# Optimization experiments

Measured on AMD Instinct MI355X. Metric: run time of the kernel, lower is better.

## Reference

```python
import jax, jax.numpy as jnp
import numpy as np

N = 16384
E = 524288
F_IN, F_HID, F_OUT = 128, 256, 128
EPS = 1e-5


def setup_inputs() -> dict:
    key = jax.random.key(0)
    ks = jax.random.split(key, 8)
    x = jax.random.normal(ks[0], (N, F_IN), dtype=jnp.float32)
    edge_index = jax.random.randint(ks[1], (2, E), 0, N, dtype=jnp.int64)
    edge_weight = jax.random.uniform(ks[2], (E,), dtype=jnp.float32)
    # Linear params stored as [in, out] (y = x @ W + b; same math as torch Linear)
    W1_w = jax.random.normal(ks[3], (F_IN, F_HID), dtype=jnp.float32) / np.sqrt(F_IN)
    W1_b = jnp.zeros((F_HID,), dtype=jnp.float32)
    W2_w = jax.random.normal(ks[4], (F_HID, F_OUT), dtype=jnp.float32) / np.sqrt(F_HID)
    W2_b = jnp.zeros((F_OUT,), dtype=jnp.float32)
    ln_g = jnp.ones((F_HID,), dtype=jnp.float32)
    ln_b = jnp.zeros((F_HID,), dtype=jnp.float32)
    return {"x": x, "edge_index": edge_index, "edge_weight": edge_weight,
            "W1_w": W1_w, "W1_b": W1_b, "W2_w": W2_w, "W2_b": W2_b,
            "ln_g": ln_g, "ln_b": ln_b}


def _layernorm(h, g, b):
    mu = jnp.mean(h, axis=-1, keepdims=True)
    var = jnp.var(h, axis=-1, keepdims=True)
    return (h - mu) * jax.lax.rsqrt(var + EPS) * g + b


def reference(x, edge_index, edge_weight, W1_w, W1_b, W2_w, W2_b, ln_g, ln_b):
    n = x.shape[0]
    adj = jnp.zeros((n, n), dtype=x.dtype).at[edge_index[0], edge_index[1]].set(edge_weight)
    adj = adj + jnp.eye(n, dtype=x.dtype)
    degree = jnp.clip(adj.sum(axis=1, keepdims=True), 1.0, None)
    adj = adj / degree
    h = jnp.matmul(adj, x) @ W1_w + W1_b          # [N, F_HID]
    h = jax.nn.relu(_layernorm(h, ln_g, ln_b))
    # dropout is identity in eval mode
    out = jnp.matmul(adj, h) @ W2_w + W2_b        # [N, F_OUT]
    return out
```

## Files before the change

### kernel.cpp

```cpp
#include <hip/hip_runtime.h>

#define N_NODES 16384
#define F_IN    128
#define F_HID   256
#define F_OUT   128
#define LN_EPS  1e-5f
#define CAP     128
#define H0STR   136
#define H1STR   264
#define REPSTR  132

typedef __attribute__((ext_vector_type(8))) short bf16x8;
typedef __attribute__((ext_vector_type(4))) float f32x4;

__device__ __forceinline__ unsigned short bf16rne(float f) {
    unsigned u = __float_as_uint(f);
    unsigned r = (u + 0x7fffu + ((u >> 16) & 1u)) >> 16;
    return (unsigned short)r;
}
__device__ __forceinline__ float bf_lo(unsigned v) { return __uint_as_float(v << 16); }
__device__ __forceinline__ float bf_hi(unsigned v) { return __uint_as_float(v & 0xffff0000u); }

__global__ void prelude_kernel(const float* __restrict__ x, unsigned short* __restrict__ xb,
                               const float* __restrict__ W1, unsigned short* __restrict__ W1t,
                               const float* __restrict__ W2, unsigned short* __restrict__ W2t,
                               int* __restrict__ cur, const unsigned* __restrict__ ei,
                               int* __restrict__ mode) {
    int b = blockIdx.x, t = threadIdx.x;
    if (b < 2048) {
        int i = (b * 256 + t) * 4;
        float4 v = *(const float4*)&x[i];
        ushort4 o;
        o.x = bf16rne(v.x); o.y = bf16rne(v.y); o.z = bf16rne(v.z); o.w = bf16rne(v.w);
        *(ushort4*)&xb[i] = o;
    } else if (b < 2176) {
        int id = (b - 2048) * 256 + t;
        int n = id >> 7, k = id & 127;
        W1t[id] = bf16rne(W1[(size_t)k * F_HID + n]);
    } else if (b < 2304) {
        int id = (b - 2176) * 256 + t;
        int n = id >> 8, k = id & 255;
        W2t[id] = bf16rne(W2[(size_t)k * F_OUT + n]);
    } else if (b < 2368) {
        cur[(b - 2304) * 256 + t] = 0;
    } else {
        __shared__ int nz;
        if (t == 0) nz = 0;
        __syncthreads();
        for (int it = 0; it < 4; ++it) {
            int idx = 2 * (t + it * 256) + 1;
            if (ei[idx] != 0u) nz = 1;
        }
        __syncthreads();
        if (t == 0) *mode = (nz == 0) ? 1 : 0;
    }
}

__global__ void fill_kernel(const void* __restrict__ ei, const int* __restrict__ mode,
                            int* __restrict__ cur, int2* __restrict__ ed, int E) {
    int base = blockIdx.x * 1024 + threadIdx.x;
    int m = *mode;
#pragma unroll
    for (int u = 0; u < 4; ++u) {
        int e = base + u * 256;
        if (e >= E) continue;
        int r, c;
        if (m) {
            const long long* p = (const long long*)ei;
            r = (int)p[e]; c = (int)p[e + E];
        } else {
            const int* p = (const int*)ei;
            r = p[e]; c = p[e + E];
        }
        if (((unsigned)r | (unsigned)c) >= N_NODES) continue;
        int pos = atomicAdd(&cur[r], 1);
        if (pos < CAP) ed[r * CAP + pos] = make_int2(c, e);
    }
}

__launch_bounds__(256)
__global__ void agg_mlp_kernel(const float* __restrict__ ew, int* __restrict__ cur,
                               int2* __restrict__ ed, float* __restrict__ invdeg,
                               const unsigned* __restrict__ xb,
                               const unsigned short* __restrict__ W1t,
                               const unsigned short* __restrict__ W2t,
                               const float* __restrict__ b1,
                               const float* __restrict__ ln_g, const float* __restrict__ ln_b,
                               unsigned short* __restrict__ h2b) {
    __shared__ int   scol[4][CAP];
    __shared__ int   seid[4][CAP];
    __shared__ float sw[4][CAP];
    __shared__ unsigned short H0[16 * H0STR];
    __shared__ unsigned short H1[16 * H1STR];
    __shared__ float red[2][4][16];

    int t = threadIdx.x, wave = t >> 6, lane = t & 63;
    int lnid = lane & 15, quad = lane >> 4;
    int Rbase = blockIdx.x * 16;

    for (int rr = 0; rr < 4; ++rr) {
        int r = Rbase + wave * 4 + rr;
        int d = cur[r];
        if (d > CAP) d = CAP;
        int2* row = ed + (size_t)r * CAP;
        for (int i = lane; i < d; i += 64) {
            int2 e = row[i];
            scol[wave][i] = e.x;
            seid[wave][i] = e.y;
        }
        __syncthreads();

        float wsum = 0.0f;
        for (int i = lane; i < d; i += 64) {
            int myc = scol[wave][i], mye = seid[wave][i];
            bool kill = false;
            for (int j = 0; j < d; ++j) {
                if (scol[wave][j] == myc) {
                    if (seid[wave][j] > mye) { kill = true; break; }
                }
            }
            float w = kill ? 0.0f : ew[mye];
            sw[wave][i] = w;
            ((int*)&row[i])[1] = __float_as_int(w);
            wsum += w;
        }
        for (int off = 32; off; off >>= 1) wsum += __shfl_xor(wsum, off, 64);
        float inv = 1.0f / (1.0f + wsum);
        if (lane == 0) { invdeg[r] = inv; cur[r] = d; }
        __syncthreads();

        unsigned self = xb[r * 64 + lane];
        float ax = bf_lo(self), ay = bf_hi(self);
        int j = 0;
        for (; j + 16 <= d; j += 16) {
            int c[16]; float w[16]; unsigned v[16];
#pragma unroll
            for (int u = 0; u < 16; ++u) { c[u] = scol[wave][j + u]; w[u] = sw[wave][j + u]; }
#pragma unroll
            for (int u = 0; u < 16; ++u) v[u] = xb[c[u] * 64 + lane];
#pragma unroll
            for (int u = 0; u < 16; ++u) { ax += w[u] * bf_lo(v[u]); ay += w[u] * bf_hi(v[u]); }
        }
        for (; j < d; ++j) {
            int cc = scol[wave][j];
            float w = sw[wave][j];
            unsigned v = xb[cc * 64 + lane];
            ax += w * bf_lo(v); ay += w * bf_hi(v);
        }
        float ox = ax * inv, oy = ay * inv;
        unsigned pack = ((unsigned)bf16rne(oy) << 16) | (unsigned)bf16rne(ox);
        *(unsigned*)&H0[(wave * 4 + rr) * H0STR + lane * 2] = pack;
    }
    __syncthreads();

    bf16x8 a[4];
#pragma unroll
    for (int ch = 0; ch < 4; ++ch)
        a[ch] = *(const bf16x8*)&H0[lnid * H0STR + ch * 32 + quad * 8];
    f32x4 acc[4];
#pragma unroll
    for (int p = 0; p < 4; ++p) {
        int ct = wave * 4 + p;
        f32x4 c = {0.0f, 0.0f, 0.0f, 0.0f};
        const unsigned short* wrow = &W1t[(size_t)(ct * 16 + lnid) * F_IN];
#pragma unroll
        for (int ch = 0; ch < 4; ++ch) {
            bf16x8 b = *(const bf16x8*)&wrow[ch * 32 + quad * 8];
            c = __builtin_amdgcn_mfma_f32_16x16x32_bf16(a[ch], b, c, 0, 0, 0);
        }
        acc[p] = c;
    }
    float s[4] = {0, 0, 0, 0}, q[4] = {0, 0, 0, 0};
#pragma unroll
    for (int p = 0; p < 4; ++p) {
        float bv = b1[(wave * 4 + p) * 16 + lnid];
#pragma unroll
        for (int r = 0; r < 4; ++r) {
            float v = acc[p][r] + bv;
            acc[p][r] = v;
            s[r] += v; q[r] += v * v;
        }
    }
#pragma unroll
    for (int r = 0; r < 4; ++r)
        for (int off = 1; off < 16; off <<= 1) {
            s[r] += __shfl_xor(s[r], off, 64);
            q[r] += __shfl_xor(q[r], off, 64);
        }
    if (lnid == 0) {
#pragma unroll
        for (int r = 0; r < 4; ++r) {
            red[0][wave][quad * 4 + r] = s[r];
            red[1][wave][quad * 4 + r] = q[r];
        }
    }
    __syncthreads();
    float mean[4], rinv[4];
#pragma unroll
    for (int r = 0; r < 4; ++r) {
        int rowi = quad * 4 + r;
        float S = red[0][0][rowi] + red[0][1][rowi] + red[0][2][rowi] + red[0][3][rowi];
        float Q = red[1][0][rowi] + red[1][1][rowi] + red[1][2][rowi] + red[1][3][rowi];
        mean[r] = S * (1.0f / F_HID);
        float var = Q * (1.0f / F_HID) - mean[r] * mean[r];
        rinv[r] = rsqrtf(var + LN_EPS);
    }
#pragma unroll
    for (int p = 0; p < 4; ++p) {
        int c = (wave * 4 + p) * 16 + lnid;
        float g = ln_g[c], bb = ln_b[c];
#pragma unroll
        for (int r = 0; r < 4; ++r) {
            float v = fmaxf((acc[p][r] - mean[r]) * rinv[r] * g + bb, 0.0f);
            H1[(quad * 4 + r) * H1STR + c] = bf16rne(v);
        }
    }
    __syncthreads();

    bf16x8 a2[8];
#pragma unroll
    for (int ch = 0; ch < 8; ++ch)
        a2[ch] = *(const bf16x8*)&H1[lnid * H1STR + ch * 32 + quad * 8];
    unsigned short* rep = H0;
#pragma unroll
    for (int p = 0; p < 2; ++p) {
        int ct = wave * 2 + p;
        f32x4 c = {0.0f, 0.0f, 0.0f, 0.0f};
        const unsigned short* wrow = &W2t[(size_t)(ct * 16 + lnid) * F_HID];
#pragma unroll
        for (int ch = 0; ch < 8; ++ch) {
            bf16x8 b = *(const bf16x8*)&wrow[ch * 32 + quad * 8];
            c = __builtin_amdgcn_mfma_f32_16x16x32_bf16(a2[ch], b, c, 0, 0, 0);
        }
#pragma unroll
        for (int r = 0; r < 4; ++r)
            rep[(quad * 4 + r) * REPSTR + ct * 16 + lnid] = bf16rne(c[r]);
    }
    __syncthreads();

#pragma unroll
    for (int p = 0; p < 2; ++p) {
        int flat = p * 256 + t;
        int m = flat >> 5, cg = flat & 31;
        *(ushort4*)&h2b[(size_t)(Rbase + m) * F_OUT + cg * 4] =
            *(const ushort4*)&rep[m * REPSTR + cg * 4];
    }
}

__global__ void spmm2_kernel(const unsigned* __restrict__ xb, const int* __restrict__ cur,
                             const int2* __restrict__ ed, const float* __restrict__ invdeg,
                             const float* __restrict__ bias, float* __restrict__ outp) {
    int wave = threadIdx.x >> 6, lane = threadIdx.x & 63;
    int r = blockIdx.x * 4 + wave;
    const int4* rowq = (const int4*)(ed + r * CAP);
    int d = cur[r];
    if (d > CAP) d = CAP;
    unsigned self = xb[r * 64 + lane];
    float ax = bf_lo(self), ay = bf_hi(self);
    int j = 0;
    for (; j + 16 <= d; j += 16) {
        int4 q[8]; int c[16]; float w[16]; unsigned v[16];
#pragma unroll
        for (int u = 0; u < 8; ++u) q[u] = rowq[(j >> 1) + u];
#pragma unroll
        for (int u = 0; u < 8; ++u) {
            c[2 * u] = q[u].x;     w[2 * u] = __int_as_float(q[u].y);
            c[2 * u + 1] = q[u].z; w[2 * u + 1] = __int_as_float(q[u].w);
        }
#pragma unroll
        for (int u = 0; u < 16; ++u) v[u] = xb[c[u] * 64 + lane];
#pragma unroll
        for (int u = 0; u < 16; ++u) { ax += w[u] * bf_lo(v[u]); ay += w[u] * bf_hi(v[u]); }
    }
    for (; j + 4 <= d; j += 4) {
        int4 q0 = rowq[j >> 1], q1 = rowq[(j >> 1) + 1];
        unsigned v0 = xb[q0.x * 64 + lane];
        unsigned v1 = xb[q0.z * 64 + lane];
        unsigned v2 = xb[q1.x * 64 + lane];
        unsigned v3 = xb[q1.z * 64 + lane];
        float w0 = __int_as_float(q0.y), w1 = __int_as_float(q0.w);
        float w2 = __int_as_float(q1.y), w3 = __int_as_float(q1.w);
        ax += w0 * bf_lo(v0) + w1 * bf_lo(v1) + w2 * bf_lo(v2) + w3 * bf_lo(v3);
        ay += w0 * bf_hi(v0) + w1 * bf_hi(v1) + w2 * bf_hi(v2) + w3 * bf_hi(v3);
    }
    const int2* row = (const int2*)(ed + r * CAP);
    for (; j < d; ++j) {
        int2 e = row[j];
        float w = __int_as_float(e.y);
        unsigned v = xb[e.x * 64 + lane];
        ax += w * bf_lo(v); ay += w * bf_hi(v);
    }
    float inv = invdeg[r];
    float ox = ax * inv + bias[2 * lane];
    float oy = ay * inv + bias[2 * lane + 1];
    ((float2*)outp)[r * 64 + lane] = make_float2(ox, oy);
}

extern "C" void kernel_launch(void* const* d_in, const int* in_sizes, int n_in,
                              void* d_out, int out_size, void* d_ws, size_t ws_size,
                              hipStream_t stream) {
    const float* x   = (const float*)d_in[0];
    const void*  ei  = d_in[1];
    const float* ew  = (const float*)d_in[2];
    const float* W1  = (const float*)d_in[3];
    const float* b1  = (const float*)d_in[4];
    const float* W2  = (const float*)d_in[5];
    const float* b2  = (const float*)d_in[6];
    const float* lng = (const float*)d_in[7];
    const float* lnb = (const float*)d_in[8];
    float* out = (float*)d_out;
    int E = in_sizes[2];

    char* w = (char*)d_ws;
    size_t off = 0;
    auto take = [&](size_t bytes) -> char* {
        char* p = w + off;
        off += (bytes + 255) & ~(size_t)255;
        return p;
    };
    int*   cur    = (int*)take((size_t)N_NODES * 4);
    float* invdeg = (float*)take((size_t)N_NODES * 4);
    int2*  ed     = (int2*)take((size_t)N_NODES * CAP * 8);
    unsigned short* xb  = (unsigned short*)take((size_t)N_NODES * F_IN * 2);
    unsigned short* h2b = (unsigned short*)take((size_t)N_NODES * F_OUT * 2);
    unsigned short* W1t = (unsigned short*)take((size_t)F_IN * F_HID * 2);
    unsigned short* W2t = (unsigned short*)take((size_t)F_HID * F_OUT * 2);
    int*   mode   = (int*)take(4);

    prelude_kernel<<<2369, 256, 0, stream>>>(x, xb, W1, W1t, W2, W2t, cur,
                                             (const unsigned*)ei, mode);
    fill_kernel<<<(E + 1023) / 1024, 256, 0, stream>>>(ei, mode, cur, ed, E);
    agg_mlp_kernel<<<N_NODES / 16, 256, 0, stream>>>(ew, cur, ed, invdeg,
                                                     (const unsigned*)xb, W1t, W2t,
                                                     b1, lng, lnb, h2b);
    spmm2_kernel<<<N_NODES / 4, 256, 0, stream>>>((const unsigned*)h2b, cur, ed, invdeg,
                                                  b2, out);
}
```

Measured before the change: 187.8 us.

## Parallelize per-row aggregation across 16 waves and split gathers into half-waves

```diff
diff --git a/kernel.cpp b/kernel.cpp
--- a/kernel.cpp
+++ b/kernel.cpp
@@ -21,28 +21,11 @@
 __device__ __forceinline__ float bf_lo(unsigned v) { return __uint_as_float(v << 16); }
 __device__ __forceinline__ float bf_hi(unsigned v) { return __uint_as_float(v & 0xffff0000u); }
 
-__global__ void prelude_kernel(const float* __restrict__ x, unsigned short* __restrict__ xb,
-                               const float* __restrict__ W1, unsigned short* __restrict__ W1t,
-                               const float* __restrict__ W2, unsigned short* __restrict__ W2t,
-                               int* __restrict__ cur, const unsigned* __restrict__ ei,
-                               int* __restrict__ mode) {
+__global__ void pre_small_kernel(int* __restrict__ cur, const unsigned* __restrict__ ei,
+                                 int* __restrict__ mode) {
     int b = blockIdx.x, t = threadIdx.x;
-    if (b < 2048) {
-        int i = (b * 256 + t) * 4;
-        float4 v = *(const float4*)&x[i];
-        ushort4 o;
-        o.x = bf16rne(v.x); o.y = bf16rne(v.y); o.z = bf16rne(v.z); o.w = bf16rne(v.w);
-        *(ushort4*)&xb[i] = o;
-    } else if (b < 2176) {
-        int id = (b - 2048) * 256 + t;
-        int n = id >> 7, k = id & 127;
-        W1t[id] = bf16rne(W1[(size_t)k * F_HID + n]);
-    } else if (b < 2304) {
-        int id = (b - 2176) * 256 + t;
-        int n = id >> 8, k = id & 255;
-        W2t[id] = bf16rne(W2[(size_t)k * F_OUT + n]);
-    } else if (b < 2368) {
-        cur[(b - 2304) * 256 + t] = 0;
+    if (b < 64) {
+        cur[b * 256 + t] = 0;
     } else {
         __shared__ int nz;
         if (t == 0) nz = 0;
@@ -56,29 +39,49 @@
     }
 }
 
-__global__ void fill_kernel(const void* __restrict__ ei, const int* __restrict__ mode,
-                            int* __restrict__ cur, int2* __restrict__ ed, int E) {
-    int base = blockIdx.x * 1024 + threadIdx.x;
-    int m = *mode;
-#pragma unroll
-    for (int u = 0; u < 4; ++u) {
-        int e = base + u * 256;
-        if (e >= E) continue;
-        int r, c;
-        if (m) {
-            const long long* p = (const long long*)ei;
-            r = (int)p[e]; c = (int)p[e + E];
-        } else {
-            const int* p = (const int*)ei;
-            r = p[e]; c = p[e + E];
-        }
-        if (((unsigned)r | (unsigned)c) >= N_NODES) continue;
-        int pos = atomicAdd(&cur[r], 1);
-        if (pos < CAP) ed[r * CAP + pos] = make_int2(c, e);
-    }
-}
-
-__launch_bounds__(256)
+__global__ void prep_fill_kernel(const void* __restrict__ ei, const int* __restrict__ mode,
+                                 int* __restrict__ cur, int2* __restrict__ ed, int E, int nF,
+                                 const float* __restrict__ x, unsigned short* __restrict__ xb,
+                                 const float* __restrict__ W1, unsigned short* __restrict__ W1t,
+                                 const float* __restrict__ W2, unsigned short* __restrict__ W2t) {
+    int b = blockIdx.x, t = threadIdx.x;
+    if (b < nF) {
+        int base = b * 1024 + t;
+        int m = *mode;
+#pragma unroll
+        for (int u = 0; u < 4; ++u) {
+            int e = base + u * 256;
+            if (e >= E) continue;
+            int r, c;
+            if (m) {
+                const long long* p = (const long long*)ei;
+                r = (int)p[e]; c = (int)p[e + E];
+            } else {
+                const int* p = (const int*)ei;
+                r = p[e]; c = p[e + E];
+            }
+            if (((unsigned)r | (unsigned)c) >= N_NODES) continue;
+            int pos = atomicAdd(&cur[r], 1);
+            if (pos < CAP) ed[r * CAP + pos] = make_int2(c, e);
+        }
+    } else if (b < nF + 2048) {
+        int i = ((b - nF) * 256 + t) * 4;
+        float4 v = *(const float4*)&x[i];
+        ushort4 o;
+        o.x = bf16rne(v.x); o.y = bf16rne(v.y); o.z = bf16rne(v.z); o.w = bf16rne(v.w);
+        *(ushort4*)&xb[i] = o;
+    } else if (b < nF + 2176) {
+        int id = (b - nF - 2048) * 256 + t;
+        int n = id >> 7, k = id & 127;
+        W1t[id] = bf16rne(W1[(size_t)k * F_HID + n]);
+    } else {
+        int id = (b - nF - 2176) * 256 + t;
+        int n = id >> 8, k = id & 255;
+        W2t[id] = bf16rne(W2[(size_t)k * F_OUT + n]);
+    }
+}
+
+__launch_bounds__(1024, 8)
 __global__ void agg_mlp_kernel(const float* __restrict__ ew, int* __restrict__ cur,
                                int2* __restrict__ ed, float* __restrict__ invdeg,
                                const unsigned* __restrict__ xb,
@@ -87,69 +90,89 @@
                                const float* __restrict__ b1,
                                const float* __restrict__ ln_g, const float* __restrict__ ln_b,
                                unsigned short* __restrict__ h2b) {
-    __shared__ int   scol[4][CAP];
-    __shared__ int   seid[4][CAP];
-    __shared__ float sw[4][CAP];
+    __shared__ int   scol[16][CAP];
+    __shared__ int   seid[16][CAP];
+    __shared__ float sw[16][CAP];
     __shared__ unsigned short H0[16 * H0STR];
     __shared__ unsigned short H1[16 * H1STR];
-    __shared__ float red[2][4][16];
+    __shared__ float red[2][16][16];
 
     int t = threadIdx.x, wave = t >> 6, lane = t & 63;
     int lnid = lane & 15, quad = lane >> 4;
+    int half = lane >> 5, hl = lane & 31;
     int Rbase = blockIdx.x * 16;
-
-    for (int rr = 0; rr < 4; ++rr) {
-        int r = Rbase + wave * 4 + rr;
-        int d = cur[r];
-        if (d > CAP) d = CAP;
-        int2* row = ed + (size_t)r * CAP;
-        for (int i = lane; i < d; i += 64) {
-            int2 e = row[i];
-            scol[wave][i] = e.x;
-            seid[wave][i] = e.y;
-        }
-        __syncthreads();
-
-        float wsum = 0.0f;
-        for (int i = lane; i < d; i += 64) {
-            int myc = scol[wave][i], mye = seid[wave][i];
-            bool kill = false;
-            for (int j = 0; j < d; ++j) {
-                if (scol[wave][j] == myc) {
-                    if (seid[wave][j] > mye) { kill = true; break; }
-                }
+    int r = Rbase + wave;
+
+    int d = cur[r];
+    if (d > CAP) d = CAP;
+    int2* row = ed + (size_t)r * CAP;
+    for (int i = lane; i < d; i += 64) {
+        int2 e = row[i];
+        scol[wave][i] = e.x;
+        seid[wave][i] = e.y;
+    }
+    asm volatile("s_waitcnt lgkmcnt(0)" ::: "memory");
+
+    float wsum = 0.0f;
+    for (int i = lane; i < d; i += 64) {
+        int myc = scol[wave][i], mye = seid[wave][i];
+        bool kill = false;
+        for (int j = 0; j < d; ++j) {
+            if (scol[wave][j] == myc) {
+                if (seid[wave][j] > mye) { kill = true; break; }
             }
-            float w = kill ? 0.0f : ew[mye];
-            sw[wave][i] = w;
-            ((int*)&row[i])[1] = __float_as_int(w);
-            wsum += w;
-        }
-        for (int off = 32; off; off >>= 1) wsum += __shfl_xor(wsum, off, 64);
-        float inv = 1.0f / (1.0f + wsum);
-        if (lane == 0) { invdeg[r] = inv; cur[r] = d; }
-        __syncthreads();
-
-        unsigned self = xb[r * 64 + lane];
-        float ax = bf_lo(self), ay = bf_hi(self);
-        int j = 0;
-        for (; j + 16 <= d; j += 16) {
-            int c[16]; float w[16]; unsigned v[16];
-#pragma unroll
-            for (int u = 0; u < 16; ++u) { c[u] = scol[wave][j + u]; w[u] = sw[wave][j + u]; }
-#pragma unroll
-            for (int u = 0; u < 16; ++u) v[u] = xb[c[u] * 64 + lane];
-#pragma unroll
-            for (int u = 0; u < 16; ++u) { ax += w[u] * bf_lo(v[u]); ay += w[u] * bf_hi(v[u]); }
-        }
-        for (; j < d; ++j) {
-            int cc = scol[wave][j];
-            float w = sw[wave][j];
-            unsigned v = xb[cc * 64 + lane];
-            ax += w * bf_lo(v); ay += w * bf_hi(v);
-        }
-        float ox = ax * inv, oy = ay * inv;
-        unsigned pack = ((unsigned)bf16rne(oy) << 16) | (unsigned)bf16rne(ox);
-        *(unsigned*)&H0[(wave * 4 + rr) * H0STR + lane * 2] = pack;
+        }
+        float w = kill ? 0.0f : ew[mye];
+        sw[wave][i] = w;
+        ((int*)&row[i])[1] = __float_as_int(w);
+        wsum += w;
+    }
+    asm volatile("s_waitcnt lgkmcnt(0)" ::: "memory");
+    for (int off = 32; off; off >>= 1) wsum += __shfl_xor(wsum, off, 64);
+    float inv = 1.0f / (1.0f + wsum);
+    if (lane == 0) { invdeg[r] = inv; cur[r] = d; }
+
+    const uint2* xb2 = (const uint2*)xb;
+    uint2 sv = xb2[(size_t)r * 32 + hl];
+    float selfw = half ? 0.0f : 1.0f;
+    float a0 = selfw * bf_lo(sv.x), a1 = selfw * bf_hi(sv.x);
+    float a2 = selfw * bf_lo(sv.y), a3 = selfw * bf_hi(sv.y);
+    int j = 0;
+    for (; j + 16 <= d; j += 16) {
+        int c[8]; float w[8]; uint2 v[8];
+#pragma unroll
+        for (int u = 0; u < 8; ++u) {
+            c[u] = scol[wave][j + 2 * u + half];
+            w[u] = sw[wave][j + 2 * u + half];
+        }
+#pragma unroll
+        for (int u = 0; u < 8; ++u) v[u] = xb2[(size_t)c[u] * 32 + hl];
+#pragma unroll
+        for (int u = 0; u < 8; ++u) {
+            a0 += w[u] * bf_lo(v[u].x); a1 += w[u] * bf_hi(v[u].x);
+            a2 += w[u] * bf_lo(v[u].y); a3 += w[u] * bf_hi(v[u].y);
+        }
+    }
+    for (; j + 2 <= d; j += 2) {
+        int cc = scol[wave][j + half];
+        float w = sw[wave][j + half];
+        uint2 v = xb2[(size_t)cc * 32 + hl];
+        a0 += w * bf_lo(v.x); a1 += w * bf_hi(v.x);
+        a2 += w * bf_lo(v.y); a3 += w * bf_hi(v.y);
+    }
+    if (j < d) {
+        int cc = scol[wave][j];
+        float w = half ? 0.0f : sw[wave][j];
+        uint2 v = xb2[(size_t)cc * 32 + hl];
+        a0 += w * bf_lo(v.x); a1 += w * bf_hi(v.x);
+        a2 += w * bf_lo(v.y); a3 += w * bf_hi(v.y);
+    }
+    a0 += __shfl_xor(a0, 32, 64); a1 += __shfl_xor(a1, 32, 64);
+    a2 += __shfl_xor(a2, 32, 64); a3 += __shfl_xor(a3, 32, 64);
+    if (half == 0) {
+        unsigned w0 = ((unsigned)bf16rne(a1 * inv) << 16) | (unsigned)bf16rne(a0 * inv);
+        unsigned w1 = ((unsigned)bf16rne(a3 * inv) << 16) | (unsigned)bf16rne(a2 * inv);
+        *(uint2*)&H0[wave * H0STR + hl * 4] = make_uint2(w0, w1);
     }
     __syncthreads();
 
@@ -157,91 +180,82 @@
 #pragma unroll
     for (int ch = 0; ch < 4; ++ch)
         a[ch] = *(const bf16x8*)&H0[lnid * H0STR + ch * 32 + quad * 8];
-    f32x4 acc[4];
-#pragma unroll
-    for (int p = 0; p < 4; ++p) {
-        int ct = wave * 4 + p;
-        f32x4 c = {0.0f, 0.0f, 0.0f, 0.0f};
-        const unsigned short* wrow = &W1t[(size_t)(ct * 16 + lnid) * F_IN];
+    f32x4 acc = {0.0f, 0.0f, 0.0f, 0.0f};
+    {
+        const unsigned short* wrow = &W1t[(size_t)(wave * 16 + lnid) * F_IN];
 #pragma unroll
         for (int ch = 0; ch < 4; ++ch) {
             bf16x8 b = *(const bf16x8*)&wrow[ch * 32 + quad * 8];
-            c = __builtin_amdgcn_mfma_f32_16x16x32_bf16(a[ch], b, c, 0, 0, 0);
-        }
-        acc[p] = c;
-    }
-    float s[4] = {0, 0, 0, 0}, q[4] = {0, 0, 0, 0};
-#pragma unroll
-    for (int p = 0; p < 4; ++p) {
-        float bv = b1[(wave * 4 + p) * 16 + lnid];
-#pragma unroll
-        for (int r = 0; r < 4; ++r) {
-            float v = acc[p][r] + bv;
-            acc[p][r] = v;
-            s[r] += v; q[r] += v * v;
-        }
-    }
-#pragma unroll
-    for (int r = 0; r < 4; ++r)
+            acc = __builtin_amdgcn_mfma_f32_16x16x32_bf16(a[ch], b, acc, 0, 0, 0);
+        }
+    }
+    float s[4], q[4];
+    {
+        float bv = b1[wave * 16 + lnid];
+#pragma unroll
+        for (int rr = 0; rr < 4; ++rr) {
+            float v = acc[rr] + bv;
+            acc[rr] = v;
+            s[rr] = v; q[rr] = v * v;
+        }
+    }
+#pragma unroll
+    for (int rr = 0; rr < 4; ++rr)
         for (int off = 1; off < 16; off <<= 1) {
-            s[r] += __shfl_xor(s[r], off, 64);
-            q[r] += __shfl_xor(q[r], off, 64);
+            s[rr] += __shfl_xor(s[rr], off, 64);
+            q[rr] += __shfl_xor(q[rr], off, 64);
         }
     if (lnid == 0) {
 #pragma unroll
-        for (int r = 0; r < 4; ++r) {
-            red[0][wave][quad * 4 + r] = s[r];
-            red[1][wave][quad * 4 + r] = q[r];
+        for (int rr = 0; rr < 4; ++rr) {
+            red[0][wave][quad * 4 + rr] = s[rr];
+            red[1][wave][quad * 4 + rr] = q[rr];
         }
     }
     __syncthreads();
     float mean[4], rinv[4];
 #pragma unroll
-    for (int r = 0; r < 4; ++r) {
-        int rowi = quad * 4 + r;
-        float S = red[0][0][rowi] + red[0][1][rowi] + red[0][2][rowi] + red[0][3][rowi];
-        float Q = red[1][0][rowi] + red[1][1][rowi] + red[1][2][rowi] + red[1][3][rowi];
-        mean[r] = S * (1.0f / F_HID);
-        float var = Q * (1.0f / F_HID) - mean[r] * mean[r];
-        rinv[r] = rsqrtf(var + LN_EPS);
-    }
-#pragma unroll
-    for (int p = 0; p < 4; ++p) {
-        int c = (wave * 4 + p) * 16 + lnid;
+    for (int rr = 0; rr < 4; ++rr) {
+        int rowi = quad * 4 + rr;
+        float S = 0.0f, Q = 0.0f;
+#pragma unroll
+        for (int w2 = 0; w2 < 16; ++w2) { S += red[0][w2][rowi]; Q += red[1][w2][rowi]; }
+        mean[rr] = S * (1.0f / F_HID);
+        float var = Q * (1.0f / F_HID) - mean[rr] * mean[rr];
+        rinv[rr] = rsqrtf(var + LN_EPS);
+    }
+    {
+        int c = wave * 16 + lnid;
         float g = ln_g[c], bb = ln_b[c];
 #pragma unroll
-        for (int r = 0; r < 4; ++r) {
-            float v = fmaxf((acc[p][r] - mean[r]) * rinv[r] * g + bb, 0.0f);
-            H1[(quad * 4 + r) * H1STR + c] = bf16rne(v);
+        for (int rr = 0; rr < 4; ++rr) {
+            float v = fmaxf((acc[rr] - mean[rr]) * rinv[rr] * g + bb, 0.0f);
+            H1[(quad * 4 + rr) * H1STR + c] = bf16rne(v);
         }
     }
     __syncthreads();
 
-    bf16x8 a2[8];
-#pragma unroll
-    for (int ch = 0; ch < 8; ++ch)
-        a2[ch] = *(const bf16x8*)&H1[lnid * H1STR + ch * 32 + quad * 8];
     unsigned short* rep = H0;
-#pragma unroll
-    for (int p = 0; p < 2; ++p) {
-        int ct = wave * 2 + p;
-        f32x4 c = {0.0f, 0.0f, 0.0f, 0.0f};
-        const unsigned short* wrow = &W2t[(size_t)(ct * 16 + lnid) * F_HID];
+    if (wave < 8) {
+        bf16x8 a2[8];
+#pragma unroll
+        for (int ch = 0; ch < 8; ++ch)
+            a2[ch] = *(const bf16x8*)&H1[lnid * H1STR + ch * 32 + quad * 8];
+        f32x4 c2 = {0.0f, 0.0f, 0.0f, 0.0f};
+        const unsigned short* wrow = &W2t[(size_t)(wave * 16 + lnid) * F_HID];
 #pragma unroll
         for (int ch = 0; ch < 8; ++ch) {
             bf16x8 b = *(const bf16x8*)&wrow[ch * 32 + quad * 8];
-            c = __builtin_amdgcn_mfma_f32_16x16x32_bf16(a2[ch], b, c, 0, 0, 0);
-        }
-#pragma unroll
-        for (int r = 0; r < 4; ++r)
-            rep[(quad * 4 + r) * REPSTR + ct * 16 + lnid] = bf16rne(c[r]);
+            c2 = __builtin_amdgcn_mfma_f32_16x16x32_bf16(a2[ch], b, c2, 0, 0, 0);
+        }
+#pragma unroll
+        for (int rr = 0; rr < 4; ++rr)
+            rep[(quad * 4 + rr) * REPSTR + wave * 16 + lnid] = bf16rne(c2[rr]);
     }
     __syncthreads();
 
-#pragma unroll
-    for (int p = 0; p < 2; ++p) {
-        int flat = p * 256 + t;
-        int m = flat >> 5, cg = flat & 31;
+    if (t < 512) {
+        int m = t >> 5, cg = t & 31;
         *(ushort4*)&h2b[(size_t)(Rbase + m) * F_OUT + cg * 4] =
             *(const ushort4*)&rep[m * REPSTR + cg * 4];
     }
@@ -251,49 +265,53 @@
                              const int2* __restrict__ ed, const float* __restrict__ invdeg,
                              const float* __restrict__ bias, float* __restrict__ outp) {
     int wave = threadIdx.x >> 6, lane = threadIdx.x & 63;
+    int half = lane >> 5, hl = lane & 31;
     int r = blockIdx.x * 4 + wave;
-    const int4* rowq = (const int4*)(ed + r * CAP);
+    const int2* row = ed + (size_t)r * CAP;
+    const uint2* xb2 = (const uint2*)xb;
     int d = cur[r];
     if (d > CAP) d = CAP;
-    unsigned self = xb[r * 64 + lane];
-    float ax = bf_lo(self), ay = bf_hi(self);
+    uint2 sv = xb2[(size_t)r * 32 + hl];
+    float selfw = half ? 0.0f : 1.0f;
+    float a0 = selfw * bf_lo(sv.x), a1 = selfw * bf_hi(sv.x);
+    float a2 = selfw * bf_lo(sv.y), a3 = selfw * bf_hi(sv.y);
     int j = 0;
     for (; j + 16 <= d; j += 16) {
-        int4 q[8]; int c[16]; float w[16]; unsigned v[16];
-#pragma unroll
-        for (int u = 0; u < 8; ++u) q[u] = rowq[(j >> 1) + u];
+        int2 q[8]; uint2 v[8];
+#pragma unroll
+        for (int u = 0; u < 8; ++u) q[u] = row[j + 2 * u + half];
+#pragma unroll
+        for (int u = 0; u < 8; ++u) v[u] = xb2[(size_t)q[u].x * 32 + hl];
 #pragma unroll
         for (int u = 0; u < 8; ++u) {
-            c[2 * u] = q[u].x;     w[2 * u] = __int_as_float(q[u].y);
-            c[2 * u + 1] = q[u].z; w[2 * u + 1] = __int_as_float(q[u].w);
-        }
-#pragma unroll
-        for (int u = 0; u < 16; ++u) v[u] = xb[c[u] * 64 + lane];
-#pragma unroll
-        for (int u = 0; u < 16; ++u) { ax += w[u] * bf_lo(v[u]); ay += w[u] * bf_hi(v[u]); }
-    }
-    for (; j + 4 <= d; j += 4) {
-        int4 q0 = rowq[j >> 1], q1 = rowq[(j >> 1) + 1];
-        unsigned v0 = xb[q0.x * 64 + lane];
-        unsigned v1 = xb[q0.z * 64 + lane];
-        unsigned v2 = xb[q1.x * 64 + lane];
-        unsigned v3 = xb[q1.z * 64 + lane];
-        float w0 = __int_as_float(q0.y), w1 = __int_as_float(q0.w);
-        float w2 = __int_as_float(q1.y), w3 = __int_as_float(q1.w);
-        ax += w0 * bf_lo(v0) + w1 * bf_lo(v1) + w2 * bf_lo(v2) + w3 * bf_lo(v3);
-        ay += w0 * bf_hi(v0) + w1 * bf_hi(v1) + w2 * bf_hi(v2) + w3 * bf_hi(v3);
-    }
-    const int2* row = (const int2*)(ed + r * CAP);
-    for (; j < d; ++j) {
-        int2 e = row[j];
-        float w = __int_as_float(e.y);
-        unsigned v = xb[e.x * 64 + lane];
-        ax += w * bf_lo(v); ay += w * bf_hi(v);
-    }
-    float inv = invdeg[r];
-    float ox = ax * inv + bias[2 * lane];
-    float oy = ay * inv + bias[2 * lane + 1];
-    ((float2*)outp)[r * 64 + lane] = make_float2(ox, oy);
+            float w = __int_as_float(q[u].y);
+            a0 += w * bf_lo(v[u].x); a1 += w * bf_hi(v[u].x);
+            a2 += w * bf_lo(v[u].y); a3 += w * bf_hi(v[u].y);
+        }
+    }
+    for (; j + 2 <= d; j += 2) {
+        int2 q = row[j + half];
+        uint2 v = xb2[(size_t)q.x * 32 + hl];
+        float w = __int_as_float(q.y);
+        a0 += w * bf_lo(v.x); a1 += w * bf_hi(v.x);
+        a2 += w * bf_lo(v.y); a3 += w * bf_hi(v.y);
+    }
+    if (j < d) {
+        int2 q = row[j];
+        float w = half ? 0.0f : __int_as_float(q.y);
+        uint2 v = xb2[(size_t)q.x * 32 + hl];
+        a0 += w * bf_lo(v.x); a1 += w * bf_hi(v.x);
+        a2 += w * bf_lo(v.y); a3 += w * bf_hi(v.y);
+    }
+    a0 += __shfl_xor(a0, 32, 64); a1 += __shfl_xor(a1, 32, 64);
+    a2 += __shfl_xor(a2, 32, 64); a3 += __shfl_xor(a3, 32, 64);
+    if (half == 0) {
+        float inv = invdeg[r];
+        float4 o;
+        o.x = a0 * inv + bias[4 * hl];     o.y = a1 * inv + bias[4 * hl + 1];
+        o.z = a2 * inv + bias[4 * hl + 2]; o.w = a3 * inv + bias[4 * hl + 3];
+        ((float4*)outp)[(size_t)r * 32 + hl] = o;
+    }
 }
 
 extern "C" void kernel_launch(void* const* d_in, const int* in_sizes, int n_in,
@@ -327,12 +345,13 @@
     unsigned short* W2t = (unsigned short*)take((size_t)F_HID * F_OUT * 2);
     int*   mode   = (int*)take(4);
 
-    prelude_kernel<<<2369, 256, 0, stream>>>(x, xb, W1, W1t, W2, W2t, cur,
-                                             (const unsigned*)ei, mode);
-    fill_kernel<<<(E + 1023) / 1024, 256, 0, stream>>>(ei, mode, cur, ed, E);
-    agg_mlp_kernel<<<N_NODES / 16, 256, 0, stream>>>(ew, cur, ed, invdeg,
-                                                     (const unsigned*)xb, W1t, W2t,
-                                                     b1, lng, lnb, h2b);
+    int nF = (E + 1023) / 1024;
+    pre_small_kernel<<<65, 256, 0, stream>>>(cur, (const unsigned*)ei, mode);
+    prep_fill_kernel<<<nF + 2304, 256, 0, stream>>>(ei, mode, cur, ed, E, nF,
+                                                    x, xb, W1, W1t, W2, W2t);
+    agg_mlp_kernel<<<N_NODES / 16, 1024, 0, stream>>>(ew, cur, ed, invdeg,
+                                                      (const unsigned*)xb, W1t, W2t,
+                                                      b1, lng, lnb, h2b);
     spmm2_kernel<<<N_NODES / 4, 256, 0, stream>>>((const unsigned*)h2b, cur, ed, invdeg,
                                                   b2, out);
 }
```

New measurement: 195.9 us. +4.3%, slower.
